# Kernel optimization log

Hardware: AMD Instinct MI355X
Metric: run time of the kernel (lower is better)

Reference implementation:

```python
import jax, jax.numpy as jnp
import numpy as np

K = 25          # kernel_size (number of B-spline control points)
DEGREE = 1      # open linear B-spline -> 2 nonzero basis weights per edge
N_NODES = 200000
N_EDGES = 6400000


def setup_inputs() -> dict:
    key = jax.random.key(0)
    k1, k2, k3, k4 = jax.random.split(key, 4)
    x = jax.random.normal(k1, (N_NODES, 2), dtype=jnp.float32)
    weight = jax.random.normal(k2, (K, 2, 1), dtype=jnp.float32)
    edges = jax.random.randint(k3, (2, N_EDGES), 0, N_NODES, dtype=jnp.int64)
    pseudo = jax.random.uniform(k4, (N_EDGES, 1), dtype=jnp.float32)
    return {"x": x, "weight": weight, "edges": edges, "pseudo": pseudo}


def reference(x, weight, edges, pseudo):
    # spline_conv with norm=True, no root_weight, no bias (forward only passes
    # x, edges, pseudo, weight, kernel_size=[25], is_open_spline=[1], degree, norm).
    row, col = edges[0], edges[1]   # messages gathered from col, scattered to row
    n = x.shape[0]

    # --- B-spline basis (open, degree 1, 1-D pseudo) ---
    p = pseudo[:, 0]                      # [E]
    v = p * (K - DEGREE)                  # [E], in [0, K-1)
    lo = jnp.floor(v)
    frac = v - lo                         # [E]
    i0 = jnp.clip(lo.astype(jnp.int32), 0, K - 1)       # [E]
    i1 = jnp.clip(i0 + 1, 0, K - 1)                     # [E]

    # --- gather + weighting: msg_e = sum_s basis[e,s] * x[col_e] @ W[idx[e,s]] ---
    xj = x[col]                                         # [E, 2]
    m0 = jnp.einsum('ef,efo->eo', xj, weight[i0])       # [E, 1]
    m1 = jnp.einsum('ef,efo->eo', xj, weight[i1])       # [E, 1]
    msg = (1.0 - frac)[:, None] * m0 + frac[:, None] * m1   # [E, 1]

    # --- scatter-add to target nodes ---
    out = jax.ops.segment_sum(msg, row, num_segments=n)     # [N, 1]

    # --- degree normalization (norm=True) ---
    deg = jax.ops.segment_sum(jnp.ones_like(p), row, num_segments=n)  # [N]
    out = out / jnp.clip(deg, 1.0, None)[:, None]
    return out
```

## Files before the change

kernel.cpp:

```cpp
#include <hip/hip_runtime.h>

#define KK 25
#define FP_SCALE 268435456.0f
#define FP_INV   (1.0f / 268435456.0f)

#define TPB 256
#define EPT 16
#define EPB (TPB * EPT)
#define WSHIFT 10
#define WNODE 1024
#define MAXBINS 256
#define CAP 36864

typedef unsigned long long u64;

__global__ void zero_counts(unsigned* __restrict__ p, int n) {
    int i = blockIdx.x * blockDim.x + threadIdx.x;
    if (i < n) p[i] = 0u;
}

__device__ __forceinline__ float2 ldg_l2(const float2* p) {
    u64 raw = __hip_atomic_load((const u64*)p, __ATOMIC_RELAXED,
                                __HIP_MEMORY_SCOPE_AGENT);
    union { u64 u; float2 f; } cv;
    cv.u = raw;
    return cv.f;
}

__global__ __launch_bounds__(TPB, 4) void phase1(
    const float* __restrict__ x,
    const float* __restrict__ w,
    const int* __restrict__ row,
    const int* __restrict__ col,
    const float* __restrict__ pseudo,
    unsigned* __restrict__ bucket,
    unsigned* __restrict__ gcount,
    int n_edges)
{
    __shared__ float4  wq[32];
    __shared__ unsigned bin_cnt[MAXBINS];
    __shared__ unsigned bin_start[MAXBINS];
    __shared__ unsigned joff[MAXBINS];
    __shared__ unsigned wtot[4];
    __shared__ unsigned stage[EPB];
    __shared__ unsigned char bin_map[EPB];

    const int tid = threadIdx.x;
    if (tid < KK) {
        int i1 = min(tid + 1, KK - 1);
        wq[tid] = make_float4(w[2 * tid], w[2 * tid + 1],
                              w[2 * i1],  w[2 * i1 + 1]);
    }
    bin_cnt[tid] = 0u;
    __syncthreads();

    const long long base = (long long)blockIdx.x * EPB;
    const bool full = (base + EPB) <= (long long)n_edges;
    const int nloc = full ? EPB
                          : (int)(((long long)n_edges - base) > 0
                                      ? ((long long)n_edges - base) : 0LL);

    unsigned entry[EPT];
    unsigned binrank[EPT];
    const float2* __restrict__ x2 = (const float2*)x;
    if (full) {
        const int4*   r4 = (const int4*)&row[base + (long long)tid * EPT];
        const int4*   c4 = (const int4*)&col[base + (long long)tid * EPT];
        const float4* p4 = (const float4*)&pseudo[base + (long long)tid * EPT];
        int4   rr[4], cc[4];
        float4 pp[4];
        #pragma unroll
        for (int q = 0; q < 4; ++q) { cc[q] = c4[q]; }
        float2 xj[16];
        #pragma unroll
        for (int q = 0; q < 4; ++q) {
            xj[4 * q + 0] = ldg_l2(&x2[cc[q].x]);
            xj[4 * q + 1] = ldg_l2(&x2[cc[q].y]);
            xj[4 * q + 2] = ldg_l2(&x2[cc[q].z]);
            xj[4 * q + 3] = ldg_l2(&x2[cc[q].w]);
        }
        #pragma unroll
        for (int q = 0; q < 4; ++q) { rr[q] = r4[q]; pp[q] = p4[q]; }
        int   ra[16];
        float pa[16];
        #pragma unroll
        for (int q = 0; q < 4; ++q) {
            ra[4 * q + 0] = rr[q].x; ra[4 * q + 1] = rr[q].y;
            ra[4 * q + 2] = rr[q].z; ra[4 * q + 3] = rr[q].w;
            pa[4 * q + 0] = pp[q].x; pa[4 * q + 1] = pp[q].y;
            pa[4 * q + 2] = pp[q].z; pa[4 * q + 3] = pp[q].w;
        }
        unsigned rk[16];
        #pragma unroll
        for (int k = 0; k < EPT; ++k) {
            int bin = ra[k] >> WSHIFT;
            rk[k] = atomicAdd(&bin_cnt[bin], 1u);
        }
        #pragma unroll
        for (int k = 0; k < EPT; ++k) {
            float vv = pa[k] * (float)(KK - 1);
            int   i0 = (int)vv;
            float fr = vv - (float)i0;
            float4 qw = wq[i0];
            float wa = qw.x + fr * (qw.z - qw.x);
            float wb = qw.y + fr * (qw.w - qw.y);
            float msg = xj[k].x * wa + xj[k].y * wb;
            unsigned ub = (__float_as_uint(msg) + 0x200u) & 0xFFFFFC00u;
            entry[k]   = ub | (unsigned)(ra[k] & (WNODE - 1));
            binrank[k] = ((unsigned)(ra[k] >> WSHIFT) << 12) | rk[k];
        }
    } else {
        for (int k = 0; k < EPT; ++k) {
            int i = tid * EPT + k;
            if (i < nloc) {
                long long e = base + i;
                int r = row[e];
                int c = col[e];
                float ps = pseudo[e];
                int bin = r >> WSHIFT;
                unsigned rank = atomicAdd(&bin_cnt[bin], 1u);
                float vv = ps * (float)(KK - 1);
                int   i0 = (int)vv;
                float fr = vv - (float)i0;
                float4 qw = wq[i0];
                float2 xj = ldg_l2(&x2[c]);
                float wa = qw.x + fr * (qw.z - qw.x);
                float wb = qw.y + fr * (qw.w - qw.y);
                float msg = xj.x * wa + xj.y * wb;
                unsigned ub = (__float_as_uint(msg) + 0x200u) & 0xFFFFFC00u;
                entry[k]   = ub | (unsigned)(r & (WNODE - 1));
                binrank[k] = ((unsigned)bin << 12) | rank;
            } else {
                binrank[k] = 0xFFFFFFFFu;
            }
        }
    }
    __syncthreads();

    {
        unsigned v = bin_cnt[tid];
        unsigned incl = v;
        #pragma unroll
        for (int d = 1; d < 64; d <<= 1) {
            unsigned t = __shfl_up(incl, d, 64);
            if ((tid & 63) >= d) incl += t;
        }
        if ((tid & 63) == 63) wtot[tid >> 6] = incl;
        __syncthreads();
        unsigned off = 0;
        const int wv = tid >> 6;
        #pragma unroll
        for (int ww = 0; ww < 4; ++ww)
            if (ww < wv) off += wtot[ww];
        unsigned st = off + incl - v;
        bin_start[tid] = st;
        unsigned gb = v ? atomicAdd(&gcount[tid], v) : 0u;
        joff[tid] = gb - st;
    }
    __syncthreads();

    if (full) {
        #pragma unroll
        for (int k = 0; k < EPT; ++k) {
            unsigned br  = binrank[k];
            unsigned bin = br >> 12;
            unsigned pos = bin_start[bin] + (br & 0xFFFu);
            stage[pos] = entry[k];
            bin_map[pos] = (unsigned char)bin;
        }
    } else {
        for (int k = 0; k < EPT; ++k) {
            unsigned br = binrank[k];
            if (br != 0xFFFFFFFFu) {
                unsigned bin = br >> 12;
                unsigned pos = bin_start[bin] + (br & 0xFFFu);
                stage[pos] = entry[k];
                bin_map[pos] = (unsigned char)bin;
            }
        }
    }
    __syncthreads();

    for (int i = tid; i < nloc; i += TPB) {
        unsigned e = stage[i];
        unsigned b = bin_map[i];
        unsigned g = joff[b] + (unsigned)i;
        if (g < CAP) bucket[(size_t)b * CAP + g] = e;
    }
}

__global__ __launch_bounds__(1024) void phase2(
    const unsigned* __restrict__ bucket,
    const unsigned* __restrict__ gcount,
    float* __restrict__ out, int n_nodes)
{
    __shared__ u64 acc[WNODE];
    const int tid = threadIdx.x;
    const int bin = blockIdx.x;

    acc[tid] = 0ULL;
    __syncthreads();

    unsigned cnt = gcount[bin];
    if (cnt > CAP) cnt = CAP;
    const unsigned* __restrict__ bb = bucket + (size_t)bin * CAP;

    const unsigned nvec = cnt >> 2;
    const uint4* __restrict__ b4 = (const uint4*)bb;
    for (unsigned i = tid; i < nvec; i += 1024) {
        uint4 e4 = b4[i];
        unsigned ee[4] = {e4.x, e4.y, e4.z, e4.w};
        #pragma unroll
        for (int j = 0; j < 4; ++j) {
            unsigned e = ee[j];
            float msg = __uint_as_float(e & 0xFFFFFC00u);
            long long fx = (long long)llrintf(msg * FP_SCALE);
            atomicAdd(&acc[e & (WNODE - 1)], ((u64)fx << 16) | 1ULL);
        }
    }
    for (unsigned i = (nvec << 2) + tid; i < cnt; i += 1024) {
        unsigned e = bb[i];
        float msg = __uint_as_float(e & 0xFFFFFC00u);
        long long fx = (long long)llrintf(msg * FP_SCALE);
        atomicAdd(&acc[e & (WNODE - 1)], ((u64)fx << 16) | 1ULL);
    }
    __syncthreads();

    const int node = (bin << WSHIFT) + tid;
    if (node < n_nodes) {
        u64 t = acc[tid];
        int count = (int)(t & 0xFFFFULL);
        long long sf = ((long long)t) >> 16;
        float sum = (float)sf * FP_INV;
        out[node] = sum / (float)max(count, 1);
    }
}

__global__ void zero_acc(u64* __restrict__ p, int n) {
    int i = blockIdx.x * blockDim.x + threadIdx.x;
    if (i < n) p[i] = 0ULL;
}

__global__ void edge_kernel_flat(const float* __restrict__ x,
                                 const float* __restrict__ w,
                                 const int* __restrict__ row,
                                 const int* __restrict__ col,
                                 const float* __restrict__ pseudo,
                                 u64* __restrict__ acc,
                                 int n_edges) {
    __shared__ float wsm[KK * 2];
    if (threadIdx.x < KK * 2) wsm[threadIdx.x] = w[threadIdx.x];
    __syncthreads();

    const float2* __restrict__ x2 = (const float2*)x;
    int e = blockIdx.x * blockDim.x + threadIdx.x;
    if (e >= n_edges) return;

    int r = row[e];
    int c = col[e];
    float p = pseudo[e];
    float vv = p * (float)(KK - 1);
    float lo = floorf(vv);
    float fr = vv - lo;
    int i0 = min(max((int)lo, 0), KK - 1);
    int i1 = min(i0 + 1, KK - 1);
    float2 xj = x2[c];
    float m0 = xj.x * wsm[2 * i0] + xj.y * wsm[2 * i0 + 1];
    float m1 = xj.x * wsm[2 * i1] + xj.y * wsm[2 * i1 + 1];
    float msg = (1.0f - fr) * m0 + fr * m1;

    long long fx = (long long)llrintf(msg * FP_SCALE);
    atomicAdd(&acc[r], ((u64)fx << 16) + 1ULL);
}

__global__ void finalize_flat(const u64* __restrict__ acc,
                              float* __restrict__ out, int n) {
    int i = blockIdx.x * blockDim.x + threadIdx.x;
    if (i >= n) return;
    u64 t = acc[i];
    int count = (int)(t & 0xFFFFULL);
    long long sf = ((long long)t) >> 16;
    float sum = (float)sf * FP_INV;
    out[i] = sum / (float)max(count, 1);
}

extern "C" void kernel_launch(void* const* d_in, const int* in_sizes, int n_in,
                              void* d_out, int out_size, void* d_ws, size_t ws_size,
                              hipStream_t stream) {
    const float* x      = (const float*)d_in[0];
    const float* w      = (const float*)d_in[1];
    const int*   edges  = (const int*)d_in[2];
    const float* pseudo = (const float*)d_in[3];

    const int n_edges = in_sizes[3];
    const int n_nodes = out_size;

    const int* row = edges;
    const int* col = edges + n_edges;

    const int nbins = (n_nodes + WNODE - 1) >> WSHIFT;
    const size_t need = 4096 + (size_t)nbins * CAP * sizeof(unsigned);

    if (nbins <= MAXBINS && ws_size >= need) {
        unsigned* gcount = (unsigned*)d_ws;
        unsigned* bucket = (unsigned*)((char*)d_ws + 4096);

        zero_counts<<<1, MAXBINS, 0, stream>>>(gcount, MAXBINS);

        int blocks = (n_edges + EPB - 1) / EPB;
        phase1<<<blocks, TPB, 0, stream>>>(x, w, row, col, pseudo,
                                           bucket, gcount, n_edges);

        phase2<<<nbins, 1024, 0, stream>>>(bucket, gcount,
                                           (float*)d_out, n_nodes);
    } else {
        u64* acc = (u64*)d_ws;
        zero_acc<<<(n_nodes + 255) / 256, 256, 0, stream>>>(acc, n_nodes);
        int blocks = (n_edges + 255) / 256;
        edge_kernel_flat<<<blocks, 256, 0, stream>>>(x, w, row, col, pseudo,
                                                     acc, n_edges);
        finalize_flat<<<(n_nodes + 255) / 256, 256, 0, stream>>>(acc,
                                                                 (float*)d_out,
                                                                 n_nodes);
    }
}
```

Before: 156.4 us.

## Split phase2 bins across four blocks and use nontemporal streaming loads/stores

Phase 2 now launches four blocks per node bin, each reducing a quarter of the bucket into shared memory and then atomically adding packed partial sums into a global accumulator, followed by a finalize kernel. With about 196 bins, this is meant to fill more of the GPU's compute units. Streaming loads of row/col/pseudo and the bucket stores and loads switch to nontemporal hints, and the x gathers go back to plain loads instead of agent-scope atomic loads. The trade-off is an extra zero kernel, an extra finalize kernel and global 64-bit atomics.

```diff
diff --git a/kernel.cpp b/kernel.cpp
--- a/kernel.cpp
+++ b/kernel.cpp
@@ -14,17 +14,31 @@
 
 typedef unsigned long long u64;
 
+typedef int      i32x4 __attribute__((ext_vector_type(4)));
+typedef float    f32x4 __attribute__((ext_vector_type(4)));
+typedef unsigned u32x4 __attribute__((ext_vector_type(4)));
+
+__device__ __forceinline__ int4 nt_load_i4(const int4* p) {
+    i32x4 v = __builtin_nontemporal_load((const i32x4*)p);
+    return make_int4(v.x, v.y, v.z, v.w);
+}
+__device__ __forceinline__ float4 nt_load_f4(const float4* p) {
+    f32x4 v = __builtin_nontemporal_load((const f32x4*)p);
+    return make_float4(v.x, v.y, v.z, v.w);
+}
+__device__ __forceinline__ uint4 nt_load_u4(const uint4* p) {
+    u32x4 v = __builtin_nontemporal_load((const u32x4*)p);
+    return make_uint4(v.x, v.y, v.z, v.w);
+}
+
 __global__ void zero_counts(unsigned* __restrict__ p, int n) {
     int i = blockIdx.x * blockDim.x + threadIdx.x;
     if (i < n) p[i] = 0u;
 }
 
-__device__ __forceinline__ float2 ldg_l2(const float2* p) {
-    u64 raw = __hip_atomic_load((const u64*)p, __ATOMIC_RELAXED,
-                                __HIP_MEMORY_SCOPE_AGENT);
-    union { u64 u; float2 f; } cv;
-    cv.u = raw;
-    return cv.f;
+__global__ void zero_acc(u64* __restrict__ p, int n) {
+    int i = blockIdx.x * blockDim.x + threadIdx.x;
+    if (i < n) p[i] = 0ULL;
 }
 
 __global__ __launch_bounds__(TPB, 4) void phase1(
@@ -70,17 +84,20 @@
         int4   rr[4], cc[4];
         float4 pp[4];
         #pragma unroll
-        for (int q = 0; q < 4; ++q) { cc[q] = c4[q]; }
+        for (int q = 0; q < 4; ++q) { cc[q] = nt_load_i4(&c4[q]); }
         float2 xj[16];
         #pragma unroll
         for (int q = 0; q < 4; ++q) {
-            xj[4 * q + 0] = ldg_l2(&x2[cc[q].x]);
-            xj[4 * q + 1] = ldg_l2(&x2[cc[q].y]);
-            xj[4 * q + 2] = ldg_l2(&x2[cc[q].z]);
-            xj[4 * q + 3] = ldg_l2(&x2[cc[q].w]);
-        }
-        #pragma unroll
-        for (int q = 0; q < 4; ++q) { rr[q] = r4[q]; pp[q] = p4[q]; }
+            xj[4 * q + 0] = x2[cc[q].x];
+            xj[4 * q + 1] = x2[cc[q].y];
+            xj[4 * q + 2] = x2[cc[q].z];
+            xj[4 * q + 3] = x2[cc[q].w];
+        }
+        #pragma unroll
+        for (int q = 0; q < 4; ++q) {
+            rr[q] = nt_load_i4(&r4[q]);
+            pp[q] = nt_load_f4(&p4[q]);
+        }
         int   ra[16];
         float pa[16];
         #pragma unroll
@@ -123,7 +140,7 @@
                 int   i0 = (int)vv;
                 float fr = vv - (float)i0;
                 float4 qw = wq[i0];
-                float2 xj = ldg_l2(&x2[c]);
+                float2 xj = x2[c];
                 float wa = qw.x + fr * (qw.z - qw.x);
                 float wb = qw.y + fr * (qw.w - qw.y);
                 float msg = xj.x * wa + xj.y * wb;
@@ -185,7 +202,58 @@
         unsigned e = stage[i];
         unsigned b = bin_map[i];
         unsigned g = joff[b] + (unsigned)i;
-        if (g < CAP) bucket[(size_t)b * CAP + g] = e;
+        if (g < CAP)
+            __builtin_nontemporal_store(e, &bucket[(size_t)b * CAP + g]);
+    }
+}
+
+__global__ __launch_bounds__(1024) void phase2_split(
+    const unsigned* __restrict__ bucket,
+    const unsigned* __restrict__ gcount,
+    u64* __restrict__ gacc, int n_nodes)
+{
+    __shared__ u64 acc[WNODE];
+    const int tid = threadIdx.x;
+    const int bin = blockIdx.x >> 2;
+    const unsigned q = (unsigned)(blockIdx.x & 3);
+
+    acc[tid] = 0ULL;
+    __syncthreads();
+
+    unsigned cnt = gcount[bin];
+    if (cnt > CAP) cnt = CAP;
+    const unsigned* __restrict__ bb = bucket + (size_t)bin * CAP;
+
+    const unsigned nvec = cnt >> 2;
+    const uint4* __restrict__ b4 = (const uint4*)bb;
+    const unsigned lo = (nvec * q) >> 2;
+    const unsigned hi = (nvec * (q + 1)) >> 2;
+
+    for (unsigned i = lo + tid; i < hi; i += 1024) {
+        uint4 e4 = nt_load_u4(&b4[i]);
+        unsigned ee[4] = {e4.x, e4.y, e4.z, e4.w};
+        #pragma unroll
+        for (int j = 0; j < 4; ++j) {
+            unsigned e = ee[j];
+            float msg = __uint_as_float(e & 0xFFFFFC00u);
+            long long fx = (long long)llrintf(msg * FP_SCALE);
+            atomicAdd(&acc[e & (WNODE - 1)], ((u64)fx << 16) | 1ULL);
+        }
+    }
+    if (q == 3) {
+        for (unsigned i = (nvec << 2) + tid; i < cnt; i += 1024) {
+            unsigned e = bb[i];
+            float msg = __uint_as_float(e & 0xFFFFFC00u);
+            long long fx = (long long)llrintf(msg * FP_SCALE);
+            atomicAdd(&acc[e & (WNODE - 1)], ((u64)fx << 16) | 1ULL);
+        }
+    }
+    __syncthreads();
+
+    const int node = (bin << WSHIFT) + tid;
+    if (node < n_nodes) {
+        u64 v = acc[tid];
+        if (v) atomicAdd(&gacc[node], v);
     }
 }
 
@@ -208,7 +276,7 @@
     const unsigned nvec = cnt >> 2;
     const uint4* __restrict__ b4 = (const uint4*)bb;
     for (unsigned i = tid; i < nvec; i += 1024) {
-        uint4 e4 = b4[i];
+        uint4 e4 = nt_load_u4(&b4[i]);
         unsigned ee[4] = {e4.x, e4.y, e4.z, e4.w};
         #pragma unroll
         for (int j = 0; j < 4; ++j) {
@@ -234,11 +302,6 @@
         float sum = (float)sf * FP_INV;
         out[node] = sum / (float)max(count, 1);
     }
-}
-
-__global__ void zero_acc(u64* __restrict__ p, int n) {
-    int i = blockIdx.x * blockDim.x + threadIdx.x;
-    if (i < n) p[i] = 0ULL;
 }
 
 __global__ void edge_kernel_flat(const float* __restrict__ x,
@@ -299,20 +362,34 @@
     const int* col = edges + n_edges;
 
     const int nbins = (n_nodes + WNODE - 1) >> WSHIFT;
-    const size_t need = 4096 + (size_t)nbins * CAP * sizeof(unsigned);
+    const size_t GOFF = 4096;
+    const size_t bucket_bytes = (size_t)nbins * CAP * sizeof(unsigned);
+    const size_t need  = GOFF + bucket_bytes;
+    const size_t need2 = need + (size_t)n_nodes * sizeof(u64);
 
     if (nbins <= MAXBINS && ws_size >= need) {
         unsigned* gcount = (unsigned*)d_ws;
-        unsigned* bucket = (unsigned*)((char*)d_ws + 4096);
+        unsigned* bucket = (unsigned*)((char*)d_ws + GOFF);
+        u64*      gacc   = (u64*)((char*)d_ws + need);
+        const bool split = (ws_size >= need2);
 
         zero_counts<<<1, MAXBINS, 0, stream>>>(gcount, MAXBINS);
+        if (split)
+            zero_acc<<<(n_nodes + 255) / 256, 256, 0, stream>>>(gacc, n_nodes);
 
         int blocks = (n_edges + EPB - 1) / EPB;
         phase1<<<blocks, TPB, 0, stream>>>(x, w, row, col, pseudo,
                                            bucket, gcount, n_edges);
 
-        phase2<<<nbins, 1024, 0, stream>>>(bucket, gcount,
-                                           (float*)d_out, n_nodes);
+        if (split) {
+            phase2_split<<<nbins * 4, 1024, 0, stream>>>(bucket, gcount,
+                                                         gacc, n_nodes);
+            finalize_flat<<<(n_nodes + 255) / 256, 256, 0, stream>>>(
+                gacc, (float*)d_out, n_nodes);
+        } else {
+            phase2<<<nbins, 1024, 0, stream>>>(bucket, gcount,
+                                               (float*)d_out, n_nodes);
+        }
     } else {
         u64* acc = (u64*)d_ws;
         zero_acc<<<(n_nodes + 255) / 256, 256, 0, stream>>>(acc, n_nodes);
```

New measurement: 178.4 us. +14.0%, slower.
